# Kernel tuning notes

Measured on AMD Instinct MI355X. Metric: run time of the kernel, lower is better.

## Reference

```python
import jax, jax.numpy as jnp
import numpy as np

EMBED_DIM = 1024
NUM_HEADS = 16
HEAD_DIM = EMBED_DIM // NUM_HEADS


def setup_inputs() -> dict:
    key = jax.random.key(0)
    ks = jax.random.split(key, 9)
    B, S, D = 2, 2048, EMBED_DIM
    scale = 1.0 / np.sqrt(D)
    inp = {
        "x": jax.random.normal(ks[0], (B, S, D), dtype=jnp.float32),
        "w_q": jax.random.normal(ks[1], (D, D), dtype=jnp.float32) * scale,
        "b_q": jnp.zeros((D,), dtype=jnp.float32),
        "w_k": jax.random.normal(ks[2], (D, D), dtype=jnp.float32) * scale,
        "b_k": jnp.zeros((D,), dtype=jnp.float32),
        "w_v": jax.random.normal(ks[3], (D, D), dtype=jnp.float32) * scale,
        "b_v": jnp.zeros((D,), dtype=jnp.float32),
        "w_o": jax.random.normal(ks[4], (D, D), dtype=jnp.float32) * scale,
        "b_o": jnp.zeros((D,), dtype=jnp.float32),
    }
    return inp


def reference(x, w_q, b_q, w_k, b_k, w_v, b_v, w_o, b_o):
    B, S, D = x.shape
    H, Hd = NUM_HEADS, HEAD_DIM

    def proj(w, b):
        # (B,S,D) @ (D,D) -> (B,S,D) -> (B,H,S,Hd)
        y = jnp.einsum('bsd,df->bsf', x, w) + b
        return y.reshape(B, S, H, Hd).transpose(0, 2, 1, 3)

    q = proj(w_q, b_q)
    k = proj(w_k, b_k)
    v = proj(w_v, b_v)

    scores = jnp.einsum('bhqd,bhkd->bhqk', q, k) / jnp.sqrt(jnp.float32(Hd))
    attn = jax.nn.softmax(scores, axis=-1)
    context = jnp.einsum('bhqk,bhkd->bhqd', attn, v)
    context = context.transpose(0, 2, 1, 3).reshape(B, S, D)
    return jnp.einsum('bsd,df->bsf', context + x, w_o) + b_o
```

## Files before the change

### kernel.cpp

```cpp
#include <hip/hip_runtime.h>
#include <hip/hip_bf16.h>

typedef _Float16 f16;
typedef _Float16 f16x8 __attribute__((ext_vector_type(8)));
typedef _Float16 f16x4 __attribute__((ext_vector_type(4)));
typedef float f32x4 __attribute__((ext_vector_type(4)));

#define EMBED 1024
#define NHEAD 16
#define HDIM 64
#define SEQ 2048
#define BATCH 2
#define NROW (BATCH * SEQ)
#define PSTR 72
#define MBIAS 14.4269504089f
#define QSCALE 0.1803368801f

__device__ __forceinline__ void gld_lds16(const f16* g, f16* l) {
    __builtin_amdgcn_global_load_lds(
        (const __attribute__((address_space(1))) void*)g,
        (__attribute__((address_space(3))) void*)l, 16, 0, 0);
}

__global__ void k_conv_x(const float* __restrict__ x, f16* __restrict__ xb) {
    int i = (blockIdx.x * blockDim.x + threadIdx.x) * 4;
    float4 v = *(const float4*)&x[i];
    f16x4 o = {(f16)v.x, (f16)v.y, (f16)v.z, (f16)v.w};
    *(f16x4*)&xb[i] = o;
}

__global__ void k_transpose4(const float* __restrict__ wq, const float* __restrict__ wk,
                             const float* __restrict__ wv, const float* __restrict__ wo,
                             f16* __restrict__ wqkvt, f16* __restrict__ wot) {
    const float* W;
    f16* Wt;
    switch (blockIdx.z) {
        case 0: W = wq; Wt = wqkvt; break;
        case 1: W = wk; Wt = wqkvt + 1024 * 1024; break;
        case 2: W = wv; Wt = wqkvt + 2 * 1024 * 1024; break;
        default: W = wo; Wt = wot; break;
    }
    __shared__ float t[32][33];
    int tx = threadIdx.x & 31, ty = threadIdx.x >> 5;
    int r0 = blockIdx.y * 32, c0 = blockIdx.x * 32;
    for (int j = 0; j < 4; ++j)
        t[ty + j * 8][tx] = W[(r0 + ty + j * 8) * 1024 + c0 + tx];
    __syncthreads();
    for (int j = 0; j < 4; ++j)
        Wt[(c0 + ty + j * 8) * 1024 + r0 + tx] = (f16)t[tx][ty + j * 8];
}

__global__ void k_bias(const float* __restrict__ bq, const float* __restrict__ bk,
                       const float* __restrict__ bv, float* __restrict__ bias) {
    int i = blockIdx.x * blockDim.x + threadIdx.x;
    if (i < 3072) bias[i] = (i < 1024) ? bq[i] : ((i < 2048) ? bk[i - 1024] : bv[i - 2048]);
}

template <bool SWAP>
__device__ __forceinline__ void gemm_kloop(const f16* __restrict__ A, const f16* __restrict__ Bt,
                                           int K, f16* Al, f16* Bl, int m0, int n0,
                                           int w, int quad, int l16, int mw, int nw,
                                           int crow, int ccol, f32x4 (&acc)[4][4]) {
    for (int k0 = 0; k0 < K; k0 += 32) {
        __syncthreads();
        gld_lds16(&A[(m0 + crow) * K + k0 + ccol], &Al[(w * 64) * 8]);
        gld_lds16(&A[(m0 + 64 + crow) * K + k0 + ccol], &Al[(256 + w * 64) * 8]);
        gld_lds16(&Bt[(n0 + crow) * K + k0 + ccol], &Bl[(w * 64) * 8]);
        gld_lds16(&Bt[(n0 + 64 + crow) * K + k0 + ccol], &Bl[(256 + w * 64) * 8]);
        __syncthreads();
        f16x8 af[4], bf[4];
        for (int i = 0; i < 4; ++i)
            af[i] = *(const f16x8*)&Al[(mw + i * 16 + l16) * 32 + quad * 8];
        for (int j = 0; j < 4; ++j)
            bf[j] = *(const f16x8*)&Bl[(nw + j * 16 + l16) * 32 + quad * 8];
        for (int i = 0; i < 4; ++i)
            for (int j = 0; j < 4; ++j)
                acc[i][j] = SWAP
                    ? __builtin_amdgcn_mfma_f32_16x16x32_f16(bf[j], af[i], acc[i][j], 0, 0, 0)
                    : __builtin_amdgcn_mfma_f32_16x16x32_f16(af[i], bf[j], acc[i][j], 0, 0, 0);
    }
}

__global__ __launch_bounds__(256) void k_gemm_qkv(const f16* __restrict__ A, const f16* __restrict__ Bt,
                                                  const float* __restrict__ bias,
                                                  f16* __restrict__ qk, f16* __restrict__ Vt) {
    __shared__ __align__(16) f16 Al[128 * 32];
    __shared__ __align__(16) f16 Bl[128 * 32];
    const int K = 1024;
    int tid = threadIdx.x;
    int w = tid >> 6, lane = tid & 63, quad = lane >> 4, l16 = lane & 15;
    int m0 = blockIdx.x * 128, n0 = blockIdx.y * 128;
    int mw = (w >> 1) * 64, nw = (w & 1) * 64;
    int c = w * 64 + lane;
    int crow = c >> 2, ccol = (c & 3) * 8;
    f32x4 acc[4][4] = {};

    if (n0 >= 2048) {
        gemm_kloop<true>(A, Bt, K, Al, Bl, m0, n0, w, quad, l16, mw, nw, crow, ccol, acc);
        for (int i = 0; i < 4; ++i) {
            int mrow = m0 + mw + i * 16 + l16;
            int b = mrow >> 11, s = mrow & 2047;
            for (int j = 0; j < 4; ++j)
                for (int r = 0; r < 4; ++r) {
                    int col = n0 + nw + j * 16 + quad * 4 + r;
                    int d = col - 2048;
                    Vt[(b * 1024 + d) * SEQ + s] = (f16)(acc[i][j][r] + bias[col]);
                }
        }
    } else {
        gemm_kloop<false>(A, Bt, K, Al, Bl, m0, n0, w, quad, l16, mw, nw, crow, ccol, acc);
        for (int i = 0; i < 4; ++i) {
            int row = m0 + mw + i * 16 + quad * 4;
            for (int j = 0; j < 4; ++j) {
                int col = n0 + nw + j * 16 + l16;
                float bval = bias[col];
                for (int r = 0; r < 4; ++r)
                    qk[(row + r) * 2048 + col] = (f16)(acc[i][j][r] + bval);
            }
        }
    }
}

__global__ __launch_bounds__(256) void k_gemm_out(const f16* __restrict__ A, const f16* __restrict__ Bt,
                                                  const float* __restrict__ bias, float* __restrict__ Cout) {
    __shared__ __align__(16) f16 Al[128 * 32];
    __shared__ __align__(16) f16 Bl[64 * 32];
    const int K = 1024, N = 1024;
    int tid = threadIdx.x;
    int w = tid >> 6, lane = tid & 63, quad = lane >> 4, l16 = lane & 15;
    int m0 = blockIdx.x * 128, n0 = blockIdx.y * 64;
    int mw = (w >> 1) * 64, nw = (w & 1) * 32;
    int c = w * 64 + lane;
    int crow = c >> 2, ccol = (c & 3) * 8;
    f32x4 acc[4][2] = {};

    for (int k0 = 0; k0 < K; k0 += 32) {
        __syncthreads();
        gld_lds16(&A[(m0 + crow) * K + k0 + ccol], &Al[(w * 64) * 8]);
        gld_lds16(&A[(m0 + 64 + crow) * K + k0 + ccol], &Al[(256 + w * 64) * 8]);
        gld_lds16(&Bt[(n0 + crow) * K + k0 + ccol], &Bl[(w * 64) * 8]);
        __syncthreads();
        f16x8 af[4], bf[2];
        for (int i = 0; i < 4; ++i)
            af[i] = *(const f16x8*)&Al[(mw + i * 16 + l16) * 32 + quad * 8];
        for (int j = 0; j < 2; ++j)
            bf[j] = *(const f16x8*)&Bl[(nw + j * 16 + l16) * 32 + quad * 8];
        for (int i = 0; i < 4; ++i)
            for (int j = 0; j < 2; ++j)
                acc[i][j] = __builtin_amdgcn_mfma_f32_16x16x32_f16(af[i], bf[j], acc[i][j], 0, 0, 0);
    }

    for (int i = 0; i < 4; ++i) {
        int row = m0 + mw + i * 16 + quad * 4;
        for (int j = 0; j < 2; ++j) {
            int col = n0 + nw + j * 16 + l16;
            float bval = bias[col];
            for (int r = 0; r < 4; ++r)
                Cout[(row + r) * N + col] = acc[i][j][r] + bval;
        }
    }
}

__global__ __launch_bounds__(256) void k_attn(const f16* __restrict__ qk, const f16* __restrict__ Vt,
                                              const float* __restrict__ x, f16* __restrict__ ctx) {
    __shared__ __align__(16) f16 Kl[64 * PSTR];
    __shared__ __align__(16) f16 Vl[64 * PSTR];
    __shared__ __align__(16) f16 Pl[4 * 32 * PSTR];

    int tid = threadIdx.x;
    int w = tid >> 6, lane = tid & 63, quad = lane >> 4, l16 = lane & 15;
    int q0 = blockIdx.x * 128;
    int bh = blockIdx.y, b = bh >> 4, h = bh & 15;
    int kbase = 1024 + h * 64;
    int qcol = h * 64;
    int vbase = b * 1024 + h * 64;
    int qw = q0 + w * 32;

    f16* Plw = &Pl[w * 32 * PSTR];

    f16x8 qf[2][2];
    for (int qg = 0; qg < 2; ++qg) {
        int qrow = b * SEQ + qw + qg * 16 + l16;
        qf[qg][0] = *(const f16x8*)&qk[qrow * 2048 + qcol + quad * 8];
        qf[qg][1] = *(const f16x8*)&qk[qrow * 2048 + qcol + 32 + quad * 8];
        for (int e = 0; e < 8; ++e) {
            qf[qg][0][e] = (f16)((float)qf[qg][0][e] * QSCALE);
            qf[qg][1][e] = (f16)((float)qf[qg][1][e] * QSCALE);
        }
    }

    int srow = (tid * 8) >> 6, scol = (tid * 8) & 63;
    const f16* kg0 = &qk[(b * SEQ + srow) * 2048 + kbase + scol];
    const f16* kg1 = kg0 + 32 * 2048;
    const f16* vg0 = &Vt[(vbase + srow) * SEQ + scol];
    const f16* vg1 = vg0 + 32 * SEQ;
    f16* kl0 = &Kl[srow * PSTR + scol];
    f16* kl1 = &Kl[(srow + 32) * PSTR + scol];
    f16* vl0 = &Vl[srow * PSTR + scol];
    f16* vl1 = &Vl[(srow + 32) * PSTR + scol];

    f32x4 oacc[2][4] = {};
    float li[2] = {0.f, 0.f};

    for (int kt = 0; kt < SEQ / 64; ++kt) {
        __syncthreads();
        *(f16x8*)kl0 = *(const f16x8*)kg0;
        *(f16x8*)kl1 = *(const f16x8*)kg1;
        *(f16x8*)vl0 = *(const f16x8*)vg0;
        *(f16x8*)vl1 = *(const f16x8*)vg1;
        kg0 += 64 * 2048; kg1 += 64 * 2048;
        vg0 += 64;        vg1 += 64;
        __syncthreads();

        f32x4 st[2][4];
        for (int nt = 0; nt < 4; ++nt) {
            f16x8 kf0 = *(const f16x8*)&Kl[(nt * 16 + l16) * PSTR + quad * 8];
            f16x8 kf1 = *(const f16x8*)&Kl[(nt * 16 + l16) * PSTR + 32 + quad * 8];
            for (int qg = 0; qg < 2; ++qg) {
                f32x4 s = {};
                s = __builtin_amdgcn_mfma_f32_16x16x32_f16(kf0, qf[qg][0], s, 0, 0, 0);
                s = __builtin_amdgcn_mfma_f32_16x16x32_f16(kf1, qf[qg][1], s, 0, 0, 0);
                st[qg][nt] = s;
            }
        }

        for (int qg = 0; qg < 2; ++qg) {
            float rs = 0.f;
            for (int nt = 0; nt < 4; ++nt)
                for (int r = 0; r < 4; ++r) {
                    float p = __builtin_amdgcn_exp2f(st[qg][nt][r] - MBIAS);
                    st[qg][nt][r] = p;
                    rs += p;
                }
            rs += __shfl_xor(rs, 16);
            rs += __shfl_xor(rs, 32);
            li[qg] += rs;
            for (int nt = 0; nt < 4; ++nt) {
                f16x4 pk;
                for (int r = 0; r < 4; ++r) pk[r] = (f16)st[qg][nt][r];
                *(f16x4*)&Plw[(qg * 16 + l16) * PSTR + nt * 16 + quad * 4] = pk;
            }
        }
        asm volatile("s_waitcnt lgkmcnt(0)" ::: "memory");

        f16x8 pf[2][2];
        for (int qg = 0; qg < 2; ++qg) {
            pf[qg][0] = *(const f16x8*)&Plw[(qg * 16 + l16) * PSTR + quad * 8];
            pf[qg][1] = *(const f16x8*)&Plw[(qg * 16 + l16) * PSTR + 32 + quad * 8];
        }
        for (int nt = 0; nt < 4; ++nt) {
            f16x8 vf0 = *(const f16x8*)&Vl[(nt * 16 + l16) * PSTR + quad * 8];
            f16x8 vf1 = *(const f16x8*)&Vl[(nt * 16 + l16) * PSTR + 32 + quad * 8];
            for (int qg = 0; qg < 2; ++qg) {
                oacc[qg][nt] = __builtin_amdgcn_mfma_f32_16x16x32_f16(pf[qg][0], vf0, oacc[qg][nt], 0, 0, 0);
                oacc[qg][nt] = __builtin_amdgcn_mfma_f32_16x16x32_f16(pf[qg][1], vf1, oacc[qg][nt], 0, 0, 0);
            }
        }
    }

    for (int qg = 0; qg < 2; ++qg) {
        float lr[4];
        for (int r = 0; r < 4; ++r) lr[r] = __shfl(li[qg], quad * 4 + r);
        for (int nt = 0; nt < 4; ++nt)
            for (int r = 0; r < 4; ++r) {
                int g = b * SEQ + qw + qg * 16 + quad * 4 + r;
                int col = h * 64 + nt * 16 + l16;
                float v = oacc[qg][nt][r] / lr[r];
                ctx[g * 1024 + col] = (f16)(v + x[g * 1024 + col]);
            }
    }
}

extern "C" void kernel_launch(void* const* d_in, const int* in_sizes, int n_in,
                              void* d_out, int out_size, void* d_ws, size_t ws_size,
                              hipStream_t stream) {
    const float* x  = (const float*)d_in[0];
    const float* wq = (const float*)d_in[1];
    const float* bq = (const float*)d_in[2];
    const float* wk = (const float*)d_in[3];
    const float* bk = (const float*)d_in[4];
    const float* wv = (const float*)d_in[5];
    const float* bv = (const float*)d_in[6];
    const float* wo = (const float*)d_in[7];
    const float* bo = (const float*)d_in[8];
    float* out = (float*)d_out;

    char* ws = (char*)d_ws;
    f16*   xb    = (f16*)(ws);
    f16*   wqkvt = (f16*)(ws + (8u << 20));
    f16*   wot   = (f16*)(ws + (14u << 20));
    float* biasq = (float*)(ws + (16u << 20));
    f16*   qkbuf = (f16*)(ws + (16u << 20) + (64u << 10));
    f16*   vtbuf = (f16*)(ws + (32u << 20) + (64u << 10));
    f16*   ctx   = xb;

    k_conv_x<<<dim3(NROW * EMBED / 1024), 256, 0, stream>>>(x, xb);
    k_transpose4<<<dim3(32, 32, 4), 256, 0, stream>>>(wq, wk, wv, wo, wqkvt, wot);
    k_bias<<<12, 256, 0, stream>>>(bq, bk, bv, biasq);

    k_gemm_qkv<<<dim3(32, 24), 256, 0, stream>>>(xb, wqkvt, biasq, qkbuf, vtbuf);
    k_attn<<<dim3(SEQ / 128, BATCH * NHEAD), 256, 0, stream>>>(qkbuf, vtbuf, x, ctx);
    k_gemm_out<<<dim3(32, 16), 256, 0, stream>>>(ctx, wot, bo, out);
}
```

Measured before the change: 239.3 us.

## Split attention keys across waves with per-wave LDS and cross-wave reduction

The attention kernel now gives each block 64 queries and has each of its four waves handle a separate quarter of the key sequence with its own private K/V/P LDS region. This removes the block-wide __syncthreads in the key loop. Partial outputs and row sums are combined through LDS at the end, and the residual add is done with vectorized stores. Separately, the x conversion and weight transposes are merged into one prep launch. The trade-off is more registers (4 query groups per wave) and a final reduction pass, and the max-free softmax with a fixed bias is kept from before.

```diff
diff --git a/kernel.cpp b/kernel.cpp
--- a/kernel.cpp
+++ b/kernel.cpp
@@ -13,6 +13,7 @@
 #define BATCH 2
 #define NROW (BATCH * SEQ)
 #define PSTR 72
+#define WBYTES (2 * 64 * PSTR * 2)
 #define MBIAS 14.4269504089f
 #define QSCALE 0.1803368801f
 
@@ -22,16 +23,17 @@
         (__attribute__((address_space(3))) void*)l, 16, 0, 0);
 }
 
-__global__ void k_conv_x(const float* __restrict__ x, f16* __restrict__ xb) {
-    int i = (blockIdx.x * blockDim.x + threadIdx.x) * 4;
-    float4 v = *(const float4*)&x[i];
-    f16x4 o = {(f16)v.x, (f16)v.y, (f16)v.z, (f16)v.w};
-    *(f16x4*)&xb[i] = o;
-}
-
-__global__ void k_transpose4(const float* __restrict__ wq, const float* __restrict__ wk,
-                             const float* __restrict__ wv, const float* __restrict__ wo,
-                             f16* __restrict__ wqkvt, f16* __restrict__ wot) {
+__global__ void k_prep(const float* __restrict__ wq, const float* __restrict__ wk,
+                       const float* __restrict__ wv, const float* __restrict__ wo,
+                       const float* __restrict__ x,
+                       f16* __restrict__ wqkvt, f16* __restrict__ wot, f16* __restrict__ xb) {
+    if (blockIdx.z >= 4) {
+        int i = (((blockIdx.z - 4) * 1024 + blockIdx.y * 32 + blockIdx.x) * 256 + threadIdx.x) * 4;
+        float4 v = *(const float4*)&x[i];
+        f16x4 o = {(f16)v.x, (f16)v.y, (f16)v.z, (f16)v.w};
+        *(f16x4*)&xb[i] = o;
+        return;
+    }
     const float* W;
     f16* Wt;
     switch (blockIdx.z) {
@@ -161,75 +163,72 @@
     }
 }
 
-__global__ __launch_bounds__(256) void k_attn(const f16* __restrict__ qk, const f16* __restrict__ Vt,
-                                              const float* __restrict__ x, f16* __restrict__ ctx) {
-    __shared__ __align__(16) f16 Kl[64 * PSTR];
-    __shared__ __align__(16) f16 Vl[64 * PSTR];
-    __shared__ __align__(16) f16 Pl[4 * 32 * PSTR];
+__global__ __launch_bounds__(256, 2) void k_attn(const f16* __restrict__ qk, const f16* __restrict__ Vt,
+                                                 const float* __restrict__ x, f16* __restrict__ ctx) {
+    __shared__ __align__(16) char smem[4 * WBYTES];
 
     int tid = threadIdx.x;
     int w = tid >> 6, lane = tid & 63, quad = lane >> 4, l16 = lane & 15;
-    int q0 = blockIdx.x * 128;
+    int q0 = blockIdx.x * 64;
     int bh = blockIdx.y, b = bh >> 4, h = bh & 15;
     int kbase = 1024 + h * 64;
     int qcol = h * 64;
     int vbase = b * 1024 + h * 64;
-    int qw = q0 + w * 32;
-
-    f16* Plw = &Pl[w * 32 * PSTR];
-
-    f16x8 qf[2][2];
-    for (int qg = 0; qg < 2; ++qg) {
-        int qrow = b * SEQ + qw + qg * 16 + l16;
-        qf[qg][0] = *(const f16x8*)&qk[qrow * 2048 + qcol + quad * 8];
-        qf[qg][1] = *(const f16x8*)&qk[qrow * 2048 + qcol + 32 + quad * 8];
-        for (int e = 0; e < 8; ++e) {
-            qf[qg][0][e] = (f16)((float)qf[qg][0][e] * QSCALE);
-            qf[qg][1][e] = (f16)((float)qf[qg][1][e] * QSCALE);
-        }
-    }
-
-    int srow = (tid * 8) >> 6, scol = (tid * 8) & 63;
-    const f16* kg0 = &qk[(b * SEQ + srow) * 2048 + kbase + scol];
-    const f16* kg1 = kg0 + 32 * 2048;
-    const f16* vg0 = &Vt[(vbase + srow) * SEQ + scol];
-    const f16* vg1 = vg0 + 32 * SEQ;
-    f16* kl0 = &Kl[srow * PSTR + scol];
-    f16* kl1 = &Kl[(srow + 32) * PSTR + scol];
-    f16* vl0 = &Vl[srow * PSTR + scol];
-    f16* vl1 = &Vl[(srow + 32) * PSTR + scol];
-
-    f32x4 oacc[2][4] = {};
-    float li[2] = {0.f, 0.f};
-
-    for (int kt = 0; kt < SEQ / 64; ++kt) {
-        __syncthreads();
-        *(f16x8*)kl0 = *(const f16x8*)kg0;
-        *(f16x8*)kl1 = *(const f16x8*)kg1;
-        *(f16x8*)vl0 = *(const f16x8*)vg0;
-        *(f16x8*)vl1 = *(const f16x8*)vg1;
-        kg0 += 64 * 2048; kg1 += 64 * 2048;
-        vg0 += 64;        vg1 += 64;
-        __syncthreads();
-
-        f32x4 st[2][4];
-        for (int nt = 0; nt < 4; ++nt) {
-            f16x8 kf0 = *(const f16x8*)&Kl[(nt * 16 + l16) * PSTR + quad * 8];
-            f16x8 kf1 = *(const f16x8*)&Kl[(nt * 16 + l16) * PSTR + 32 + quad * 8];
-            for (int qg = 0; qg < 2; ++qg) {
+
+    f16* Kw = (f16*)(smem + w * WBYTES);
+    f16* Vw = Kw + 64 * PSTR;
+    f16* Pw = Kw;
+
+    f16x8 qf[4][2];
+    for (int qg = 0; qg < 4; ++qg) {
+        int qrow = b * SEQ + q0 + qg * 16 + l16;
+        for (int kk = 0; kk < 2; ++kk) {
+            f16x8 v = *(const f16x8*)&qk[qrow * 2048 + qcol + kk * 32 + quad * 8];
+            for (int e = 0; e < 8; ++e) v[e] = (f16)((float)v[e] * QSCALE);
+            qf[qg][kk] = v;
+        }
+    }
+
+    int srow = lane >> 3;
+    int scol = (lane & 7) * 8;
+    const f16* kgp = &qk[(b * SEQ + w * 512 + srow) * 2048 + kbase + scol];
+    const f16* vgp = &Vt[(vbase + srow) * SEQ + w * 512 + scol];
+
+    f32x4 oacc[4][4] = {};
+    float li[4] = {0.f, 0.f, 0.f, 0.f};
+
+    for (int kt = 0; kt < 8; ++kt) {
+        f16x8 tk[8], tv[8];
+        for (int c = 0; c < 8; ++c) {
+            tk[c] = *(const f16x8*)(kgp + c * 8 * 2048);
+            tv[c] = *(const f16x8*)(vgp + c * 8 * SEQ);
+        }
+        kgp += 64 * 2048;
+        vgp += 64;
+        for (int c = 0; c < 8; ++c) {
+            *(f16x8*)&Kw[(c * 8 + srow) * PSTR + scol] = tk[c];
+            *(f16x8*)&Vw[(c * 8 + srow) * PSTR + scol] = tv[c];
+        }
+
+        f16x8 kf[4][2];
+        for (int nt = 0; nt < 4; ++nt)
+            for (int kk = 0; kk < 2; ++kk)
+                kf[nt][kk] = *(const f16x8*)&Kw[(nt * 16 + l16) * PSTR + kk * 32 + quad * 8];
+        asm volatile("s_waitcnt lgkmcnt(0)" ::: "memory");
+
+        for (int qg = 0; qg < 4; ++qg) {
+            f32x4 st[4];
+            for (int nt = 0; nt < 4; ++nt) {
                 f32x4 s = {};
-                s = __builtin_amdgcn_mfma_f32_16x16x32_f16(kf0, qf[qg][0], s, 0, 0, 0);
-                s = __builtin_amdgcn_mfma_f32_16x16x32_f16(kf1, qf[qg][1], s, 0, 0, 0);
-                st[qg][nt] = s;
+                s = __builtin_amdgcn_mfma_f32_16x16x32_f16(kf[nt][0], qf[qg][0], s, 0, 0, 0);
+                s = __builtin_amdgcn_mfma_f32_16x16x32_f16(kf[nt][1], qf[qg][1], s, 0, 0, 0);
+                st[nt] = s;
             }
-        }
-
-        for (int qg = 0; qg < 2; ++qg) {
             float rs = 0.f;
             for (int nt = 0; nt < 4; ++nt)
                 for (int r = 0; r < 4; ++r) {
-                    float p = __builtin_amdgcn_exp2f(st[qg][nt][r] - MBIAS);
-                    st[qg][nt][r] = p;
+                    float p = __builtin_amdgcn_exp2f(st[nt][r] - MBIAS);
+                    st[nt][r] = p;
                     rs += p;
                 }
             rs += __shfl_xor(rs, 16);
@@ -237,38 +236,64 @@
             li[qg] += rs;
             for (int nt = 0; nt < 4; ++nt) {
                 f16x4 pk;
-                for (int r = 0; r < 4; ++r) pk[r] = (f16)st[qg][nt][r];
-                *(f16x4*)&Plw[(qg * 16 + l16) * PSTR + nt * 16 + quad * 4] = pk;
+                for (int r = 0; r < 4; ++r) pk[r] = (f16)st[nt][r];
+                *(f16x4*)&Pw[(qg * 16 + l16) * PSTR + nt * 16 + quad * 4] = pk;
             }
         }
         asm volatile("s_waitcnt lgkmcnt(0)" ::: "memory");
 
-        f16x8 pf[2][2];
-        for (int qg = 0; qg < 2; ++qg) {
-            pf[qg][0] = *(const f16x8*)&Plw[(qg * 16 + l16) * PSTR + quad * 8];
-            pf[qg][1] = *(const f16x8*)&Plw[(qg * 16 + l16) * PSTR + 32 + quad * 8];
-        }
+        f16x8 pf[4][2];
+        for (int qg = 0; qg < 4; ++qg)
+            for (int kk = 0; kk < 2; ++kk)
+                pf[qg][kk] = *(const f16x8*)&Pw[(qg * 16 + l16) * PSTR + kk * 32 + quad * 8];
         for (int nt = 0; nt < 4; ++nt) {
-            f16x8 vf0 = *(const f16x8*)&Vl[(nt * 16 + l16) * PSTR + quad * 8];
-            f16x8 vf1 = *(const f16x8*)&Vl[(nt * 16 + l16) * PSTR + 32 + quad * 8];
-            for (int qg = 0; qg < 2; ++qg) {
+            f16x8 vf0 = *(const f16x8*)&Vw[(nt * 16 + l16) * PSTR + quad * 8];
+            f16x8 vf1 = *(const f16x8*)&Vw[(nt * 16 + l16) * PSTR + 32 + quad * 8];
+            for (int qg = 0; qg < 4; ++qg) {
                 oacc[qg][nt] = __builtin_amdgcn_mfma_f32_16x16x32_f16(pf[qg][0], vf0, oacc[qg][nt], 0, 0, 0);
                 oacc[qg][nt] = __builtin_amdgcn_mfma_f32_16x16x32_f16(pf[qg][1], vf1, oacc[qg][nt], 0, 0, 0);
             }
         }
     }
 
-    for (int qg = 0; qg < 2; ++qg) {
-        float lr[4];
-        for (int r = 0; r < 4; ++r) lr[r] = __shfl(li[qg], quad * 4 + r);
+    __syncthreads();
+    float* Ow = (float*)(smem + w * WBYTES);
+    float* Lw = (float*)(smem + w * WBYTES + 16384);
+    for (int qg = 0; qg < 4; ++qg)
         for (int nt = 0; nt < 4; ++nt)
-            for (int r = 0; r < 4; ++r) {
-                int g = b * SEQ + qw + qg * 16 + quad * 4 + r;
-                int col = h * 64 + nt * 16 + l16;
-                float v = oacc[qg][nt][r] / lr[r];
-                ctx[g * 1024 + col] = (f16)(v + x[g * 1024 + col]);
-            }
-    }
+            for (int r = 0; r < 4; ++r)
+                Ow[(qg * 16 + quad * 4 + r) * 64 + nt * 16 + l16] = oacc[qg][nt][r];
+    if (quad == 0)
+        for (int qg = 0; qg < 4; ++qg) Lw[qg * 16 + l16] = li[qg];
+    __syncthreads();
+
+    int q = tid >> 2, d0 = (tid & 3) * 16;
+    f32x4 a4[4] = {};
+    float lsum = 0.f;
+    for (int w2 = 0; w2 < 4; ++w2) {
+        const float* Ow2 = (const float*)(smem + w2 * WBYTES);
+        const float* Lw2 = (const float*)(smem + w2 * WBYTES + 16384);
+        for (int j = 0; j < 4; ++j)
+            a4[j] += *(const f32x4*)&Ow2[q * 64 + d0 + 4 * j];
+        lsum += Lw2[q];
+    }
+    int g = b * SEQ + q0 + q;
+    int cb = h * 64 + d0;
+    float inv = 1.f / lsum;
+    f16x8 o0, o1;
+    for (int j = 0; j < 4; ++j) {
+        float4 xv = *(const float4*)&x[g * 1024 + cb + 4 * j];
+        float4 r;
+        r.x = a4[j][0] * inv + xv.x;
+        r.y = a4[j][1] * inv + xv.y;
+        r.z = a4[j][2] * inv + xv.z;
+        r.w = a4[j][3] * inv + xv.w;
+        f16* dst = (j < 2) ? (f16*)&o0 : (f16*)&o1;
+        int o = (j & 1) * 4;
+        dst[o + 0] = (f16)r.x; dst[o + 1] = (f16)r.y; dst[o + 2] = (f16)r.z; dst[o + 3] = (f16)r.w;
+    }
+    *(f16x8*)&ctx[g * 1024 + cb] = o0;
+    *(f16x8*)&ctx[g * 1024 + cb + 8] = o1;
 }
 
 extern "C" void kernel_launch(void* const* d_in, const int* in_sizes, int n_in,
@@ -294,11 +319,10 @@
     f16*   vtbuf = (f16*)(ws + (32u << 20) + (64u << 10));
     f16*   ctx   = xb;
 
-    k_conv_x<<<dim3(NROW * EMBED / 1024), 256, 0, stream>>>(x, xb);
-    k_transpose4<<<dim3(32, 32, 4), 256, 0, stream>>>(wq, wk, wv, wo, wqkvt, wot);
+    k_prep<<<dim3(32, 32, 8), 256, 0, stream>>>(wq, wk, wv, wo, x, wqkvt, wot, xb);
     k_bias<<<12, 256, 0, stream>>>(bq, bk, bv, biasq);
 
     k_gemm_qkv<<<dim3(32, 24), 256, 0, stream>>>(xb, wqkvt, biasq, qkbuf, vtbuf);
-    k_attn<<<dim3(SEQ / 128, BATCH * NHEAD), 256, 0, stream>>>(qkbuf, vtbuf, x, ctx);
+    k_attn<<<dim3(SEQ / 64, BATCH * NHEAD), 256, 0, stream>>>(qkbuf, vtbuf, x, ctx);
     k_gemm_out<<<dim3(32, 16), 256, 0, stream>>>(ctx, wot, bo, out);
 }
```

Result: faster. 216.8 us (-9.4%).
